# Kernel optimization log

Measured on AMD Instinct MI355X. Metric: run time of the kernel, lower is better.

Reference implementation:

```python
import jax, jax.numpy as jnp
import numpy as np

jax.config.update("jax_enable_x64", True)

NUM_PARTS = 4
N_CAD = 8192
N_CAM = 8192


def setup_inputs() -> dict:
    key = jax.random.key(0)
    ks = jax.random.split(key, 7)
    cad_pts = jax.random.normal(ks[0], (NUM_PARTS, N_CAD, 3), jnp.float32)
    camera_pts = jax.random.normal(ks[1], (NUM_PARTS, N_CAM, 3), jnp.float32)
    part_weight = jax.random.uniform(ks[2], (NUM_PARTS,), jnp.float32)
    rot_quats = jax.random.normal(ks[3], (NUM_PARTS, 4), jnp.float32)  # [w,x,y,z] per part
    tras = 0.1 * jax.random.normal(ks[4], (NUM_PARTS, 3, 1), jnp.float32)
    rt_k = jnp.eye(4, dtype=jnp.float32)[None] + 0.01 * jax.random.normal(ks[5], (NUM_PARTS, 4, 4), jnp.float32)
    joint_axes = jax.random.normal(ks[6], (NUM_PARTS - 1, 2, 4), jnp.float32)
    return {"camera_pts": camera_pts, "cad_pts": cad_pts, "part_weight": part_weight,
            "rot_quats": rot_quats, "tras": tras, "rt_k": rt_k, "joint_axes": joint_axes}


def _quat_to_rot(q):
    # q = [w, x, y, z] -> a,b,c,d as in the torch code
    q = q / jnp.linalg.norm(q)
    a, b, c, d = q[0], q[1], q[2], q[3]
    return jnp.stack([
        1 - 2 * c * c - 2 * d * d, 2 * b * c - 2 * a * d, 2 * a * c + 2 * b * d,
        2 * b * c + 2 * a * d, 1 - 2 * b * b - 2 * d * d, 2 * c * d - 2 * a * b,
        2 * b * d - 2 * a * c, 2 * a * b + 2 * c * d, 1 - 2 * b * b - 2 * c * c,
    ]).reshape(3, 3)


def _chamfer(x, y):
    # symmetric Chamfer (mean of k=1 NN distances both ways), in float64 like torch code
    x = x.astype(jnp.float64)
    y = y.astype(jnp.float64)
    x2 = jnp.sum(x * x, axis=1)  # [N]
    y2 = jnp.sum(y * y, axis=1)  # [M]
    d2 = x2[:, None] + y2[None, :] - 2.0 * (x @ y.T)  # [N,M]
    d = jnp.sqrt(jnp.maximum(d2, 0.0))
    return jnp.min(d, axis=1).mean() + jnp.min(d, axis=0).mean()


def _forward(camera_pts, cad_pts, part_weight, rot_quats, tras, rt_k, joint_axes):
    P = cad_pts.shape[0]
    f32 = jnp.float32
    # homogeneous coords [P,N,4] / [P,M,4]
    scad = jnp.concatenate([cad_pts, jnp.ones(cad_pts.shape[:2] + (1,), f32)], axis=-1)
    scam = jnp.concatenate([camera_pts, jnp.ones(camera_pts.shape[:2] + (1,), f32)], axis=-1)

    rots = jax.vmap(_quat_to_rot)(rot_quats)                       # [P,3,3]
    top = jnp.concatenate([rots, tras], axis=2)                    # [P,3,4]
    bottom = jnp.broadcast_to(jnp.array([[[0.0, 0.0, 0.0, 1.0]]], f32), (P, 1, 4))
    transforms = jnp.concatenate([top, bottom], axis=1)            # [P,4,4]

    cad_base = jnp.einsum('pij,pnj->pni', transforms, scad)        # [P,N,4]
    e_geo = jax.vmap(_chamfer)(cad_base, scam)                     # [P] float64
    eners = 5.0 * e_geo                                            # [P]

    # torch.tensor(eners) detaches -> stop_gradient
    et = jax.lax.stop_gradient(eners)
    et = (et - jnp.min(et)) / (jnp.max(et) - jnp.min(et) + 1e-8)
    sm = jax.nn.softmax(et, axis=0)                                # [P] float64

    errors_p = part_weight.astype(jnp.float64) * sm * eners        # [P]
    all_obj = jnp.sum(sm * eners)

    # ---- E_kin ----
    x_t = jnp.einsum('pij,pnj->pni', transforms, scad)             # [P,N,4]
    distances = jnp.linalg.norm(x_t - scam, axis=-1).mean(axis=-1).mean()
    Tj_q = rt_k[0] @ transforms[0] @ joint_axes[0, 0]              # [4] (fixed index 0, as in source)
    Tj1_q = jnp.einsum('pij,pjk,pk->pi', rt_k[1:], transforms[1:], joint_axes[:, 1])  # [P-1,4]
    diff = (Tj_q[None, :] - Tj1_q)[:, :3]                          # [P-1,3]
    nrm = jnp.linalg.norm(diff) / P
    e_kin = jnp.log(0.1 * nrm + 1.0) + distances

    e_kin_total = jnp.max(errors_p) * e_kin
    all_obj = all_obj + e_kin_total
    errors = jnp.concatenate([errors_p, e_kin_total[None]])        # [P+1]
    return all_obj, errors, jax.lax.stop_gradient(transforms)


def reference(camera_pts, cad_pts, part_weight, rot_quats, tras, rt_k, joint_axes):
    return _forward(camera_pts, cad_pts, part_weight, rot_quats, tras, rt_k, joint_axes)
```

## Files before the change

kernel.cpp:

```cpp
#include <hip/hip_runtime.h>
#include <cstdint>
#include <math.h>

#define NPARTS 4
#define NPTS   8192

#define WS_SUMS_OFF 256
#define WS_MIN_OFF  384

typedef float f32x2 __attribute__((ext_vector_type(2)));
typedef float f32x4 __attribute__((ext_vector_type(4)));

__device__ __forceinline__ f32x2 pk_fma(f32x2 a, f32x2 b, f32x2 c) {
    f32x2 d;
    asm("v_pk_fma_f32 %0, %1, %2, %3" : "=v"(d) : "v"(a), "v"(b), "v"(c));
    return d;
}
__device__ __forceinline__ float min3f(float a, float b, float c) {
    float d;
    asm("v_min3_f32 %0, %1, %2, %3" : "=v"(d) : "v"(a), "v"(b), "v"(c));
    return d;
}

__global__ __launch_bounds__(256) void k_setup(const float* __restrict__ rot_quats,
                                               const float* __restrict__ tras,
                                               float* __restrict__ ws,
                                               float* __restrict__ out) {
    uint32_t* minbuf = (uint32_t*)((char*)ws + WS_MIN_OFF);
    int gid = blockIdx.x * blockDim.x + threadIdx.x;
    int nthr = gridDim.x * blockDim.x;
    for (int i = gid; i < 2 * NPARTS * NPTS; i += nthr) minbuf[i] = 0x7F800000u;
    if (blockIdx.x == 0) {
        if (threadIdx.x >= 16 && threadIdx.x < 25) {
            double* s = (double*)((char*)ws + WS_SUMS_OFF);
            s[threadIdx.x - 16] = 0.0;
        }
        if (threadIdx.x < NPARTS) {
            int p = threadIdx.x;
            double q0 = rot_quats[p*4+0], q1 = rot_quats[p*4+1];
            double q2 = rot_quats[p*4+2], q3 = rot_quats[p*4+3];
            double inv = 1.0 / sqrt(q0*q0 + q1*q1 + q2*q2 + q3*q3);
            double a = q0*inv, b = q1*inv, c = q2*inv, d = q3*inv;
            float T[16];
            T[0]  = (float)(1.0 - 2.0*c*c - 2.0*d*d);
            T[1]  = (float)(2.0*b*c - 2.0*a*d);
            T[2]  = (float)(2.0*a*c + 2.0*b*d);
            T[3]  = tras[p*3+0];
            T[4]  = (float)(2.0*b*c + 2.0*a*d);
            T[5]  = (float)(1.0 - 2.0*b*b - 2.0*d*d);
            T[6]  = (float)(2.0*c*d - 2.0*a*b);
            T[7]  = tras[p*3+1];
            T[8]  = (float)(2.0*b*d - 2.0*a*c);
            T[9]  = (float)(2.0*a*b + 2.0*c*d);
            T[10] = (float)(1.0 - 2.0*b*b - 2.0*c*c);
            T[11] = tras[p*3+2];
            T[12] = 0.f; T[13] = 0.f; T[14] = 0.f; T[15] = 1.f;
            #pragma unroll
            for (int i = 0; i < 16; ++i) {
                ws[p*16 + i] = T[i];
                out[6 + p*16 + i] = T[i];
            }
        }
    }
}

__global__ __launch_bounds__(256, 4) void k_chamfer(const float* __restrict__ cam,
                                                    const float* __restrict__ cad,
                                                    float* __restrict__ ws) {
    constexpr int TPB = 256, REG_X = 8;
    constexpr int XTILE = TPB * REG_X;
    constexpr int XTILES = NPTS / XTILE;
    constexpr int YSPLIT = 32;
    constexpr int YLEN = NPTS / YSPLIT;
    __shared__ f32x4 ybuf4[4][YLEN / 4];

    uint32_t* minbuf = (uint32_t*)((char*)ws + WS_MIN_OFF);

    int b   = blockIdx.x;
    int ysi = b & (YSPLIT - 1);
    int xt  = (b / YSPLIT) & (XTILES - 1);
    int dir = (b / (YSPLIT * XTILES)) & 1;
    int p   = b / (YSPLIT * XTILES * 2);

    float T[12];
    #pragma unroll
    for (int i = 0; i < 12; ++i) T[i] = ws[p*16 + i];

    const float* xsrc = (dir == 0) ? cad + (size_t)p*NPTS*3 : cam + (size_t)p*NPTS*3;
    const float* ysrc = (dir == 0) ? cam + (size_t)p*NPTS*3 : cad + (size_t)p*NPTS*3;

    {
        int j = threadIdx.x;
        int yi = ysi * YLEN + j;
        float v0 = ysrc[yi*3+0], v1 = ysrc[yi*3+1], v2 = ysrc[yi*3+2];
        if (dir == 1) {
            float w0 = T[0]*v0 + T[1]*v1 + T[2]*v2 + T[3];
            float w1 = T[4]*v0 + T[5]*v1 + T[6]*v2 + T[7];
            float w2 = T[8]*v0 + T[9]*v1 + T[10]*v2 + T[11];
            v0 = w0; v1 = w1; v2 = w2;
        }
        ((float*)ybuf4[0])[j] = -2.f * v0;
        ((float*)ybuf4[1])[j] = -2.f * v1;
        ((float*)ybuf4[2])[j] = -2.f * v2;
        ((float*)ybuf4[3])[j] = v0*v0 + v1*v1 + v2*v2;
    }

    f32x2 x0pk[REG_X], x1pk[REG_X], x2pk[REG_X];
    #pragma unroll
    for (int r = 0; r < REG_X; ++r) {
        int xi = xt*XTILE + r*TPB + threadIdx.x;
        float v0 = xsrc[xi*3+0], v1 = xsrc[xi*3+1], v2 = xsrc[xi*3+2];
        if (dir == 0) {
            float w0 = T[0]*v0 + T[1]*v1 + T[2]*v2 + T[3];
            float w1 = T[4]*v0 + T[5]*v1 + T[6]*v2 + T[7];
            float w2 = T[8]*v0 + T[9]*v1 + T[10]*v2 + T[11];
            v0 = w0; v1 = w1; v2 = w2;
        }
        x0pk[r] = (f32x2){v0, v0};
        x1pk[r] = (f32x2){v1, v1};
        x2pk[r] = (f32x2){v2, v2};
    }

    float mn[REG_X];
    #pragma unroll
    for (int r = 0; r < REG_X; ++r) mn[r] = INFINITY;

    __syncthreads();

    for (int g = 0; g < YLEN / 4; ++g) {
        f32x4 c0 = ybuf4[0][g];
        f32x4 c1 = ybuf4[1][g];
        f32x4 c2 = ybuf4[2][g];
        f32x4 qq = ybuf4[3][g];
        f32x2 c0lo = __builtin_shufflevector(c0, c0, 0, 1), c0hi = __builtin_shufflevector(c0, c0, 2, 3);
        f32x2 c1lo = __builtin_shufflevector(c1, c1, 0, 1), c1hi = __builtin_shufflevector(c1, c1, 2, 3);
        f32x2 c2lo = __builtin_shufflevector(c2, c2, 0, 1), c2hi = __builtin_shufflevector(c2, c2, 2, 3);
        f32x2 qqlo = __builtin_shufflevector(qq, qq, 0, 1), qqhi = __builtin_shufflevector(qq, qq, 2, 3);
        #pragma unroll
        for (int r = 0; r < REG_X; ++r) {
            f32x2 t = pk_fma(x0pk[r], c0lo, qqlo);
            t = pk_fma(x1pk[r], c1lo, t);
            t = pk_fma(x2pk[r], c2lo, t);
            mn[r] = min3f(mn[r], t.x, t.y);
            f32x2 u = pk_fma(x0pk[r], c0hi, qqhi);
            u = pk_fma(x1pk[r], c1hi, u);
            u = pk_fma(x2pk[r], c2hi, u);
            mn[r] = min3f(mn[r], u.x, u.y);
        }
    }

    #pragma unroll
    for (int r = 0; r < REG_X; ++r) {
        int xi = xt*XTILE + r*TPB + threadIdx.x;
        float v0 = x0pk[r].x, v1 = x1pk[r].x, v2 = x2pk[r].x;
        float d2 = fmaxf(v0*v0 + v1*v1 + v2*v2 + mn[r], 0.f);
        atomicMin(&minbuf[(dir*NPARTS + p)*NPTS + xi], __float_as_uint(d2));
    }
}

__global__ __launch_bounds__(256) void k_reduce(const float* __restrict__ cam,
                                                const float* __restrict__ cad,
                                                float* __restrict__ ws) {
    __shared__ double red[256];
    double local = 0.0;
    int b = blockIdx.x;
    if (b < 64) {
        uint32_t* minbuf = (uint32_t*)((char*)ws + WS_MIN_OFF);
        int base = b * 1024;
        #pragma unroll
        for (int k = 0; k < 4; ++k) {
            uint32_t bits = minbuf[base + k*256 + threadIdx.x];
            local += sqrt((double)__uint_as_float(bits));
        }
        red[threadIdx.x] = local;
        __syncthreads();
        for (int s = 128; s > 0; s >>= 1) {
            if (threadIdx.x < s) red[threadIdx.x] += red[threadIdx.x + s];
            __syncthreads();
        }
        if (threadIdx.x == 0) {
            double* sums = (double*)((char*)ws + WS_SUMS_OFF);
            int dir = b >> 5;
            int p = (b >> 3) & 3;
            atomicAdd(&sums[p*2 + dir], red[0]);
        }
    } else {
        int gid = (b - 64) * 256 + threadIdx.x;
        int p = gid >> 13;
        float T[12];
        #pragma unroll
        for (int i = 0; i < 12; ++i) T[i] = ws[p*16 + i];
        float v0 = cad[gid*3+0], v1 = cad[gid*3+1], v2 = cad[gid*3+2];
        float w0 = T[0]*v0 + T[1]*v1 + T[2]*v2 + T[3];
        float w1 = T[4]*v0 + T[5]*v1 + T[6]*v2 + T[7];
        float w2 = T[8]*v0 + T[9]*v1 + T[10]*v2 + T[11];
        float d0 = w0 - cam[gid*3+0];
        float d1 = w1 - cam[gid*3+1];
        float d2 = w2 - cam[gid*3+2];
        local = sqrt((double)(d0*d0 + d1*d1 + d2*d2));
        red[threadIdx.x] = local;
        __syncthreads();
        for (int s = 128; s > 0; s >>= 1) {
            if (threadIdx.x < s) red[threadIdx.x] += red[threadIdx.x + s];
            __syncthreads();
        }
        if (threadIdx.x == 0) {
            double* dist_sum = (double*)((char*)ws + WS_SUMS_OFF) + 8;
            atomicAdd(dist_sum, red[0]);
        }
    }
}

__global__ void k_final(const float* __restrict__ pw,
                        const float* __restrict__ rtk,
                        const float* __restrict__ ja,
                        const float* __restrict__ ws,
                        float* __restrict__ out) {
    const double* sums = (const double*)((const char*)ws + WS_SUMS_OFF);
    double eners[NPARTS];
    for (int p = 0; p < NPARTS; ++p)
        eners[p] = 5.0 * ((sums[p*2+0] + sums[p*2+1]) / (double)NPTS);

    double mn = eners[0], mx = eners[0];
    for (int p = 1; p < NPARTS; ++p) { mn = fmin(mn, eners[p]); mx = fmax(mx, eners[p]); }
    double et[NPARTS], etmax = -1e300;
    for (int p = 0; p < NPARTS; ++p) { et[p] = (eners[p] - mn) / (mx - mn + 1e-8); etmax = fmax(etmax, et[p]); }
    double ex[NPARTS], se = 0.0;
    for (int p = 0; p < NPARTS; ++p) { ex[p] = exp(et[p] - etmax); se += ex[p]; }

    double ep[NPARTS], all_obj = 0.0, epmax = -1e300;
    for (int p = 0; p < NPARTS; ++p) {
        double sm = ex[p] / se;
        ep[p] = (double)pw[p] * sm * eners[p];
        all_obj += sm * eners[p];
        epmax = fmax(epmax, ep[p]);
    }

    double distances = sums[8] / (double)(NPARTS * NPTS);

    double v[4], Tj[4], ss = 0.0;
    for (int i = 0; i < 4; ++i) {
        v[i] = 0.0;
        for (int k = 0; k < 4; ++k) v[i] += (double)ws[0*16 + i*4 + k] * (double)ja[0*8 + 0*4 + k];
    }
    for (int i = 0; i < 4; ++i) {
        Tj[i] = 0.0;
        for (int k = 0; k < 4; ++k) Tj[i] += (double)rtk[0*16 + i*4 + k] * v[k];
    }
    for (int q = 1; q < NPARTS; ++q) {
        double vv[4], u[4];
        for (int i = 0; i < 4; ++i) {
            vv[i] = 0.0;
            for (int k = 0; k < 4; ++k) vv[i] += (double)ws[q*16 + i*4 + k] * (double)ja[(q-1)*8 + 4 + k];
        }
        for (int i = 0; i < 4; ++i) {
            u[i] = 0.0;
            for (int k = 0; k < 4; ++k) u[i] += (double)rtk[q*16 + i*4 + k] * vv[k];
        }
        for (int i = 0; i < 3; ++i) { double dd = Tj[i] - u[i]; ss += dd * dd; }
    }
    double nrm = sqrt(ss) / (double)NPARTS;
    double e_kin = log(0.1 * nrm + 1.0) + distances;
    double ekt = epmax * e_kin;
    all_obj += ekt;

    out[0] = (float)all_obj;
    for (int p = 0; p < NPARTS; ++p) out[1 + p] = (float)ep[p];
    out[5] = (float)ekt;
}

extern "C" void kernel_launch(void* const* d_in, const int* in_sizes, int n_in,
                              void* d_out, int out_size, void* d_ws, size_t ws_size,
                              hipStream_t stream) {
    const float* cam  = (const float*)d_in[0];
    const float* cad  = (const float*)d_in[1];
    const float* pw   = (const float*)d_in[2];
    const float* rq   = (const float*)d_in[3];
    const float* tras = (const float*)d_in[4];
    const float* rtk  = (const float*)d_in[5];
    const float* ja   = (const float*)d_in[6];
    float* out = (float*)d_out;
    float* ws  = (float*)d_ws;

    hipLaunchKernelGGL(k_setup,   dim3(64),   dim3(256), 0, stream, rq, tras, ws, out);
    hipLaunchKernelGGL(k_chamfer, dim3(1024), dim3(256), 0, stream, cam, cad, ws);
    hipLaunchKernelGGL(k_reduce,  dim3(192),  dim3(256), 0, stream, cam, cad, ws);
    hipLaunchKernelGGL(k_final,   dim3(1),    dim3(1),   0, stream, pw, rtk, ja, ws, out);
}
```

Before: 55.42 us.

## Replace atomicMin chamfer merge with per-split partial slabs reduced later

The chamfer kernel now writes its per-Y-split minimum distances into separate partial slabs instead of doing atomicMin into one shared buffer. The reduce kernel takes the min across the 16 slabs before the sqrt and sum. This drops the atomics and the setup pass that initialised the min buffer to infinity, so k_setup shrinks to a single block. The Y split is halved to 16, which halves the chamfer grid to 512 blocks with longer per-block Y loops; in exchange the reduce kernel reads 16x more data.

```diff
diff --git a/kernel.cpp b/kernel.cpp
--- a/kernel.cpp
+++ b/kernel.cpp
@@ -4,9 +4,10 @@
 
 #define NPARTS 4
 #define NPTS   8192
+#define YSPLIT 16
 
 #define WS_SUMS_OFF 256
-#define WS_MIN_OFF  384
+#define WS_PART_OFF 384
 
 typedef float f32x2 __attribute__((ext_vector_type(2)));
 typedef float f32x4 __attribute__((ext_vector_type(4)));
@@ -26,40 +27,34 @@
                                                const float* __restrict__ tras,
                                                float* __restrict__ ws,
                                                float* __restrict__ out) {
-    uint32_t* minbuf = (uint32_t*)((char*)ws + WS_MIN_OFF);
-    int gid = blockIdx.x * blockDim.x + threadIdx.x;
-    int nthr = gridDim.x * blockDim.x;
-    for (int i = gid; i < 2 * NPARTS * NPTS; i += nthr) minbuf[i] = 0x7F800000u;
-    if (blockIdx.x == 0) {
-        if (threadIdx.x >= 16 && threadIdx.x < 25) {
-            double* s = (double*)((char*)ws + WS_SUMS_OFF);
-            s[threadIdx.x - 16] = 0.0;
-        }
-        if (threadIdx.x < NPARTS) {
-            int p = threadIdx.x;
-            double q0 = rot_quats[p*4+0], q1 = rot_quats[p*4+1];
-            double q2 = rot_quats[p*4+2], q3 = rot_quats[p*4+3];
-            double inv = 1.0 / sqrt(q0*q0 + q1*q1 + q2*q2 + q3*q3);
-            double a = q0*inv, b = q1*inv, c = q2*inv, d = q3*inv;
-            float T[16];
-            T[0]  = (float)(1.0 - 2.0*c*c - 2.0*d*d);
-            T[1]  = (float)(2.0*b*c - 2.0*a*d);
-            T[2]  = (float)(2.0*a*c + 2.0*b*d);
-            T[3]  = tras[p*3+0];
-            T[4]  = (float)(2.0*b*c + 2.0*a*d);
-            T[5]  = (float)(1.0 - 2.0*b*b - 2.0*d*d);
-            T[6]  = (float)(2.0*c*d - 2.0*a*b);
-            T[7]  = tras[p*3+1];
-            T[8]  = (float)(2.0*b*d - 2.0*a*c);
-            T[9]  = (float)(2.0*a*b + 2.0*c*d);
-            T[10] = (float)(1.0 - 2.0*b*b - 2.0*c*c);
-            T[11] = tras[p*3+2];
-            T[12] = 0.f; T[13] = 0.f; T[14] = 0.f; T[15] = 1.f;
-            #pragma unroll
-            for (int i = 0; i < 16; ++i) {
-                ws[p*16 + i] = T[i];
-                out[6 + p*16 + i] = T[i];
-            }
+    if (threadIdx.x >= 16 && threadIdx.x < 25) {
+        double* s = (double*)((char*)ws + WS_SUMS_OFF);
+        s[threadIdx.x - 16] = 0.0;
+    }
+    if (threadIdx.x < NPARTS) {
+        int p = threadIdx.x;
+        double q0 = rot_quats[p*4+0], q1 = rot_quats[p*4+1];
+        double q2 = rot_quats[p*4+2], q3 = rot_quats[p*4+3];
+        double inv = 1.0 / sqrt(q0*q0 + q1*q1 + q2*q2 + q3*q3);
+        double a = q0*inv, b = q1*inv, c = q2*inv, d = q3*inv;
+        float T[16];
+        T[0]  = (float)(1.0 - 2.0*c*c - 2.0*d*d);
+        T[1]  = (float)(2.0*b*c - 2.0*a*d);
+        T[2]  = (float)(2.0*a*c + 2.0*b*d);
+        T[3]  = tras[p*3+0];
+        T[4]  = (float)(2.0*b*c + 2.0*a*d);
+        T[5]  = (float)(1.0 - 2.0*b*b - 2.0*d*d);
+        T[6]  = (float)(2.0*c*d - 2.0*a*b);
+        T[7]  = tras[p*3+1];
+        T[8]  = (float)(2.0*b*d - 2.0*a*c);
+        T[9]  = (float)(2.0*a*b + 2.0*c*d);
+        T[10] = (float)(1.0 - 2.0*b*b - 2.0*c*c);
+        T[11] = tras[p*3+2];
+        T[12] = 0.f; T[13] = 0.f; T[14] = 0.f; T[15] = 1.f;
+        #pragma unroll
+        for (int i = 0; i < 16; ++i) {
+            ws[p*16 + i] = T[i];
+            out[6 + p*16 + i] = T[i];
         }
     }
 }
@@ -70,11 +65,10 @@
     constexpr int TPB = 256, REG_X = 8;
     constexpr int XTILE = TPB * REG_X;
     constexpr int XTILES = NPTS / XTILE;
-    constexpr int YSPLIT = 32;
     constexpr int YLEN = NPTS / YSPLIT;
     __shared__ f32x4 ybuf4[4][YLEN / 4];
 
-    uint32_t* minbuf = (uint32_t*)((char*)ws + WS_MIN_OFF);
+    float* partial = (float*)((char*)ws + WS_PART_OFF);
 
     int b   = blockIdx.x;
     int ysi = b & (YSPLIT - 1);
@@ -89,8 +83,7 @@
     const float* xsrc = (dir == 0) ? cad + (size_t)p*NPTS*3 : cam + (size_t)p*NPTS*3;
     const float* ysrc = (dir == 0) ? cam + (size_t)p*NPTS*3 : cad + (size_t)p*NPTS*3;
 
-    {
-        int j = threadIdx.x;
+    for (int j = threadIdx.x; j < YLEN; j += TPB) {
         int yi = ysi * YLEN + j;
         float v0 = ysrc[yi*3+0], v1 = ysrc[yi*3+1], v2 = ysrc[yi*3+2];
         if (dir == 1) {
@@ -149,12 +142,13 @@
         }
     }
 
+    float* slab = partial + (size_t)((dir*NPARTS + p)*YSPLIT + ysi) * NPTS;
     #pragma unroll
     for (int r = 0; r < REG_X; ++r) {
         int xi = xt*XTILE + r*TPB + threadIdx.x;
         float v0 = x0pk[r].x, v1 = x1pk[r].x, v2 = x2pk[r].x;
         float d2 = fmaxf(v0*v0 + v1*v1 + v2*v2 + mn[r], 0.f);
-        atomicMin(&minbuf[(dir*NPARTS + p)*NPTS + xi], __float_as_uint(d2));
+        slab[xi] = d2;
     }
 }
 
@@ -165,12 +159,19 @@
     double local = 0.0;
     int b = blockIdx.x;
     if (b < 64) {
-        uint32_t* minbuf = (uint32_t*)((char*)ws + WS_MIN_OFF);
-        int base = b * 1024;
+        const float* partial = (const float*)((const char*)ws + WS_PART_OFF);
+        int dir   = b >> 5;
+        int p     = (b >> 3) & 3;
+        int chunk = b & 7;
+        const float* base = partial + (size_t)(dir*NPARTS + p) * YSPLIT * NPTS;
         #pragma unroll
         for (int k = 0; k < 4; ++k) {
-            uint32_t bits = minbuf[base + k*256 + threadIdx.x];
-            local += sqrt((double)__uint_as_float(bits));
+            int x = chunk*1024 + k*256 + threadIdx.x;
+            float mnv = INFINITY;
+            #pragma unroll
+            for (int ysi = 0; ysi < YSPLIT; ++ysi)
+                mnv = fminf(mnv, base[(size_t)ysi*NPTS + x]);
+            local += sqrt((double)mnv);
         }
         red[threadIdx.x] = local;
         __syncthreads();
@@ -180,8 +181,6 @@
         }
         if (threadIdx.x == 0) {
             double* sums = (double*)((char*)ws + WS_SUMS_OFF);
-            int dir = b >> 5;
-            int p = (b >> 3) & 3;
             atomicAdd(&sums[p*2 + dir], red[0]);
         }
     } else {
@@ -282,8 +281,8 @@
     float* out = (float*)d_out;
     float* ws  = (float*)d_ws;
 
-    hipLaunchKernelGGL(k_setup,   dim3(64),   dim3(256), 0, stream, rq, tras, ws, out);
-    hipLaunchKernelGGL(k_chamfer, dim3(1024), dim3(256), 0, stream, cam, cad, ws);
-    hipLaunchKernelGGL(k_reduce,  dim3(192),  dim3(256), 0, stream, cam, cad, ws);
-    hipLaunchKernelGGL(k_final,   dim3(1),    dim3(1),   0, stream, pw, rtk, ja, ws, out);
-}
+    hipLaunchKernelGGL(k_setup,   dim3(1),   dim3(256), 0, stream, rq, tras, ws, out);
+    hipLaunchKernelGGL(k_chamfer, dim3(512), dim3(256), 0, stream, cam, cad, ws);
+    hipLaunchKernelGGL(k_reduce,  dim3(192), dim3(256), 0, stream, cam, cad, ws);
+    hipLaunchKernelGGL(k_final,   dim3(1),   dim3(1),   0, stream, pw, rtk, ja, ws, out);
+}
```

Result: slower. 56.64 us (+2.2%).
